# Kernel tuning notes

Measured on AMD Instinct MI355X. Metric: run time of the kernel, lower is better.

## Reference

```python
import jax, jax.numpy as jnp
import numpy as np

B, N, L, E, D = 16, 16384, 192, 128, 128


def setup_inputs() -> dict:
    key = jax.random.key(0)
    ks = jax.random.split(key, 16)
    s = 0.05
    return {
        "x_L_flattened": jax.random.normal(ks[0], (B, N), jnp.float32),
        "x_y_mask_flattened": jax.random.randint(ks[1], (B, N), 0, 2).astype(jnp.float32),
        "y_mask_L_flattened": jnp.zeros((B, N), jnp.float32),
        "x_y_mark": jax.random.normal(ks[2], (B, L, 1), jnp.float32),
        "variable_indices_flattened": jax.random.randint(ks[3], (B, N), 0, E),
        "time_indices_flattened": jax.random.randint(ks[4], (B, N), 0, L),
        "N_OBSERVATIONS_MAX": N,
        # learned params (stored [in, out]; torch Linear uses x @ W.T + b)
        "W_obs": jax.random.normal(ks[5], (2, D), jnp.float32) * s,
        "b_obs": jnp.zeros((D,), jnp.float32),
        "W_time": jax.random.normal(ks[6], (1, D), jnp.float32) * s,
        "b_time": jnp.zeros((D,), jnp.float32),
        "var_hyperedge_w": jax.random.normal(ks[7], (E, D), jnp.float32),
        "W_q": jax.random.normal(ks[8], (D, D), jnp.float32) * s,
        "b_q": jnp.zeros((D,), jnp.float32),
        "W_k": jax.random.normal(ks[9], (D, D), jnp.float32) * s,
        "b_k": jnp.zeros((D,), jnp.float32),
        "W_v": jax.random.normal(ks[10], (D, D), jnp.float32) * s,
        "b_v": jnp.zeros((D,), jnp.float32),
        "threshold": jnp.float32(0.5),
        "merge_coef": jnp.float32(0.5),
    }


def reference(x_L_flattened, x_y_mask_flattened, y_mask_L_flattened, x_y_mark,
              variable_indices_flattened, time_indices_flattened, N_OBSERVATIONS_MAX,
              W_obs, b_obs, W_time, b_time, var_hyperedge_w,
              W_q, b_q, W_k, b_k, W_v, b_v, threshold, merge_coef):
    mask = x_y_mask_flattened  # [B, N]
    # node features: value + (1 - mask + y_mask) channel -> [B, N, 2]
    feats = jnp.stack([x_L_flattened, 1.0 - mask + y_mask_L_flattened], axis=-1)
    # temporal incidence: node n belongs to time-edge l iff time_idx[n] == l; [B, L, N]
    ti = (time_indices_flattened[:, None, :] == jnp.arange(L)[None, :, None]).astype(jnp.float32)
    ti = ti * mask[:, None, :]
    # variable incidence: node n belongs to var-edge e iff var_idx[n] == e; [B, E, N]
    vi = (jnp.arange(E)[None, :, None] == variable_indices_flattened[:, None, :]).astype(jnp.float32)
    vi = vi * mask[:, None, :]
    # encoders
    obs = jax.nn.relu(feats @ W_obs + b_obs) * mask[..., None]          # [B, N, D]
    temp_he = jnp.sin(x_y_mark @ W_time + b_time)                        # [B, L, D]
    var_he = jax.nn.relu(jnp.broadcast_to(var_hyperedge_w, (B, E, D)))   # [B, E, D]
    # IrregularityAwareAttention over variable hyperedges with incidence as aux
    q = var_he @ W_q + b_q
    k = var_he @ W_k + b_k
    v = var_he @ W_v + b_v
    att = jnp.einsum('bed,bfd->bef', q, k) / (D ** 0.5)                  # [B, E, E]
    att_aux = jnp.einsum('ben,bfn->bef', vi, vi) / (N_OBSERVATIONS_MAX ** 0.5)
    merge = (att > threshold) & (att_aux != 0)
    att = jnp.where(merge, (1.0 - merge_coef) * att + merge_coef * att_aux, att)
    attn = jax.nn.softmax(att, axis=-1)
    out = jnp.einsum('bef,bfd->bed', attn, v)                            # [B, E, D]
    return (obs, temp_he, out, ti, vi)
```

## Files before the change

kernel.cpp:

```cpp
#include <hip/hip_runtime.h>

#define Bb 16
#define Nn 16384
#define Ll 192
#define Ee 128
#define Dd 128


__global__ __launch_bounds__(256) void k_main(
    const int* __restrict__ tidx, const int* __restrict__ vidx,
    const float* __restrict__ mask, const float* __restrict__ var_w,
    const float* __restrict__ Wq, const float* __restrict__ bq,
    const float* __restrict__ Wk, const float* __restrict__ bk,
    const float* __restrict__ Wv, const float* __restrict__ bv,
    const float* __restrict__ x, const float* __restrict__ ymask,
    const float* __restrict__ W_obs, const float* __restrict__ b_obs,
    const float* __restrict__ mark, const float* __restrict__ Wt,
    const float* __restrict__ bt,
    float* __restrict__ ti, float* __restrict__ vi,
    float* __restrict__ cnt_part,
    float* __restrict__ q, float* __restrict__ kT, float* __restrict__ v,
    float* __restrict__ obs, float* __restrict__ temp)
{
    __shared__ float sh[Ee];
    const int tid = threadIdx.x;

    if (blockIdx.x < 1024) {
        const int pb      = blockIdx.x >> 2;
        const int quarter = blockIdx.x & 3;
        const int g  = pb * 256 + tid;
        const int b  = g >> 12;
        const int n4 = (g & 4095) << 2;

        const int4   t4 = *reinterpret_cast<const int4*>(tidx + b * Nn + n4);
        const int4   v4 = *reinterpret_cast<const int4*>(vidx + b * Nn + n4);
        const float4 m4 = *reinterpret_cast<const float4*>(mask + b * Nn + n4);

        if (quarter == 0) {
            if (tid < Ee) sh[tid] = 0.0f;
            __syncthreads();
            if (m4.x != 0.0f) atomicAdd(&sh[v4.x], 1.0f);
            if (m4.y != 0.0f) atomicAdd(&sh[v4.y], 1.0f);
            if (m4.z != 0.0f) atomicAdd(&sh[v4.z], 1.0f);
            if (m4.w != 0.0f) atomicAdd(&sh[v4.w], 1.0f);
        }

        const int l0 = quarter * 48;
        float* tib = ti + (((size_t)b * Ll) << 14) + n4;
        #pragma unroll 4
        for (int l = l0; l < l0 + 48; ++l) {
            float4 o;
            o.x = (t4.x == l) ? m4.x : 0.0f;
            o.y = (t4.y == l) ? m4.y : 0.0f;
            o.z = (t4.z == l) ? m4.z : 0.0f;
            o.w = (t4.w == l) ? m4.w : 0.0f;
            *reinterpret_cast<float4*>(tib + ((size_t)l << 14)) = o;
        }

        const int e0 = quarter * 32;
        float* vib = vi + (((size_t)b * Ee) << 14) + n4;
        #pragma unroll 4
        for (int e = e0; e < e0 + 32; ++e) {
            float4 o;
            o.x = (v4.x == e) ? m4.x : 0.0f;
            o.y = (v4.y == e) ? m4.y : 0.0f;
            o.z = (v4.z == e) ? m4.z : 0.0f;
            o.w = (v4.w == e) ? m4.w : 0.0f;
            *reinterpret_cast<float4*>(vib + ((size_t)e << 14)) = o;
        }

        if (quarter == 0) {
            __syncthreads();
            if (tid < Ee) cnt_part[pb * Ee + tid] = sh[tid];
        }
    } else if (blockIdx.x < 1152) {
        const int e = blockIdx.x - 1024;
        const int d = tid;
        if (d < Dd) sh[d] = fmaxf(var_w[e * Dd + d], 0.0f);
        __syncthreads();
        if (d < Dd) {
            float aq = bq[d], ak = bk[d], av = bv[d];
            #pragma unroll 4
            for (int j = 0; j < Dd; ++j) {
                const float hj = sh[j];
                aq = fmaf(hj, Wq[j * Dd + d], aq);
                ak = fmaf(hj, Wk[j * Dd + d], ak);
                av = fmaf(hj, Wv[j * Dd + d], av);
            }
            q[e * Dd + d]  = aq;
            kT[d * Dd + e] = ak;
            v[e * Dd + d]  = av;
        }
    } else if (blockIdx.x < 33920) {
        const int g   = (blockIdx.x - 1152) * 256 + tid;
        const int row = g >> 5;
        const int d   = (g & 31) << 2;

        const float m  = mask[row];
        const float xv = x[row];
        const float f1 = 1.0f - m + ymask[row];

        const float4 w0 = *reinterpret_cast<const float4*>(W_obs + d);
        const float4 w1 = *reinterpret_cast<const float4*>(W_obs + Dd + d);
        const float4 bb = *reinterpret_cast<const float4*>(b_obs + d);

        float4 o;
        o.x = fmaxf(fmaf(xv, w0.x, fmaf(f1, w1.x, bb.x)), 0.0f) * m;
        o.y = fmaxf(fmaf(xv, w0.y, fmaf(f1, w1.y, bb.y)), 0.0f) * m;
        o.z = fmaxf(fmaf(xv, w0.z, fmaf(f1, w1.z, bb.z)), 0.0f) * m;
        o.w = fmaxf(fmaf(xv, w0.w, fmaf(f1, w1.w, bb.w)), 0.0f) * m;
        *reinterpret_cast<float4*>(obs + ((size_t)row << 7) + d) = o;
    } else {
        const int idx = (blockIdx.x - 33920) * 256 + tid;
        const int d = idx & 127;
        const int r = idx >> 7;
        temp[idx] = sinf(fmaf(mark[r], Wt[d], bt[d]));
    }
}

__global__ __launch_bounds__(128) void k_soft(
    const float* __restrict__ q, const float* __restrict__ kT,
    const float* __restrict__ v, const float* __restrict__ cnt_part,
    const float* __restrict__ thr_p, const float* __restrict__ mc_p,
    const int* __restrict__ nobs_p, float* __restrict__ outp)
{
    __shared__ float qr[Dd];
    __shared__ float attn[Ee];
    __shared__ float red[5];
    const int b = blockIdx.x >> 7;
    const int e = blockIdx.x & 127;
    const int f = threadIdx.x;

    qr[f] = q[e * Dd + f];

    float cp = (f < 16) ? cnt_part[(b * 16 + f) * Ee + e] : 0.0f;
    #pragma unroll
    for (int off = 8; off > 0; off >>= 1) cp += __shfl_xor(cp, off);
    if (f == 0) red[4] = cp;
    __syncthreads();

    float acc0 = 0.0f;
    #pragma unroll 4
    for (int d = 0; d < Dd; ++d) acc0 = fmaf(qr[d], kT[d * Dd + f], acc0);
    float a = acc0 * 0.08838834764831845f;

    if (f == e) {
        const float c = red[4];
        const float thr = *thr_p;
        if (c != 0.0f && a > thr) {
            const float mc  = *mc_p;
            const float aux = c / sqrtf((float)(*nobs_p));
            a = (1.0f - mc) * a + mc * aux;
        }
    }

    float mx = a;
    #pragma unroll
    for (int off = 32; off > 0; off >>= 1) mx = fmaxf(mx, __shfl_xor(mx, off));
    if ((f & 63) == 0) red[f >> 6] = mx;
    __syncthreads();
    mx = fmaxf(red[0], red[1]);

    const float ex = expf(a - mx);
    float s = ex;
    #pragma unroll
    for (int off = 32; off > 0; off >>= 1) s += __shfl_xor(s, off);
    if ((f & 63) == 0) red[2 + (f >> 6)] = s;
    __syncthreads();
    s = red[2] + red[3];

    attn[f] = ex / s;
    __syncthreads();

    const int d = f;
    float acc = 0.0f;
    #pragma unroll 4
    for (int j = 0; j < Ee; ++j) acc = fmaf(attn[j], v[j * Dd + d], acc);
    outp[((size_t)(b * Ee + e) << 7) + d] = acc;
}

extern "C" void kernel_launch(void* const* d_in, const int* in_sizes, int n_in,
                              void* d_out, int out_size, void* d_ws, size_t ws_size,
                              hipStream_t stream) {
    (void)in_sizes; (void)n_in; (void)out_size; (void)ws_size;

    const float* x      = (const float*)d_in[0];
    const float* mask   = (const float*)d_in[1];
    const float* ymask  = (const float*)d_in[2];
    const float* mark   = (const float*)d_in[3];
    const int*   vidx   = (const int*)d_in[4];
    const int*   tidx   = (const int*)d_in[5];
    const int*   nobs   = (const int*)d_in[6];
    const float* W_obs  = (const float*)d_in[7];
    const float* b_obs  = (const float*)d_in[8];
    const float* W_time = (const float*)d_in[9];
    const float* b_time = (const float*)d_in[10];
    const float* var_w  = (const float*)d_in[11];
    const float* W_q    = (const float*)d_in[12];
    const float* b_q    = (const float*)d_in[13];
    const float* W_k    = (const float*)d_in[14];
    const float* b_k    = (const float*)d_in[15];
    const float* W_v    = (const float*)d_in[16];
    const float* b_v    = (const float*)d_in[17];
    const float* thr    = (const float*)d_in[18];
    const float* mc     = (const float*)d_in[19];

    float* out_base = (float*)d_out;
    float* obs  = out_base;
    float* temp = out_base + 33554432;
    float* attO = out_base + 33947648;
    float* ti   = out_base + 34209792;
    float* vi   = out_base + 84541440;

    float* ws       = (float*)d_ws;
    float* cnt_part = ws;
    float* q        = ws + 32768;
    float* kT       = ws + 49152;
    float* v        = ws + 65536;

    k_main<<<35456, 256, 0, stream>>>(tidx, vidx, mask, var_w,
                                      W_q, b_q, W_k, b_k, W_v, b_v,
                                      x, ymask, W_obs, b_obs,
                                      mark, W_time, b_time,
                                      ti, vi, cnt_part, q, kT, v, obs, temp);
    k_soft<<<Bb * Ee, Dd, 0, stream>>>(q, kT, v, cnt_part, thr, mc, nobs, attO);
}
```

Baseline: 572.0 us.

## Replace dense one-hot incidence writes with bulk zero-fill plus sparse scatter

Instead of each thread computing and storing every compare-select entry of the ti and vi incidence matrices, the main kernel now zero-fills the contiguous ti+vi output region with wide coalesced stores. A separate scatter kernel then writes only the masked nonzero entries and computes the per-block variable counts. This aims to turn the dominant output traffic into a simple, well-parallelised memset and to spread it over many more blocks. In exchange it adds an extra kernel launch and a serial dependency, and it issues scattered 4-byte stores for the nonzeros.

Result: faster. 552.4 us (-3.4%).

```diff
diff --git a/kernel.cpp b/kernel.cpp
--- a/kernel.cpp
+++ b/kernel.cpp
@@ -7,92 +7,35 @@
 #define Dd 128
 
 
+#define QKV_NB   128
+#define TEMP_NB  1536
+#define FILL_NB  20480
+#define OBS_NB   32768
+#define TEMP_B0  (QKV_NB)
+#define FILL_B0  (TEMP_B0 + TEMP_NB)
+#define OBS_B0   (FILL_B0 + FILL_NB)
+#define GRID1    (OBS_B0 + OBS_NB)
+
 __global__ __launch_bounds__(256) void k_main(
-    const int* __restrict__ tidx, const int* __restrict__ vidx,
-    const float* __restrict__ mask, const float* __restrict__ var_w,
+    const float* __restrict__ var_w,
     const float* __restrict__ Wq, const float* __restrict__ bq,
     const float* __restrict__ Wk, const float* __restrict__ bk,
     const float* __restrict__ Wv, const float* __restrict__ bv,
-    const float* __restrict__ x, const float* __restrict__ ymask,
+    const float* __restrict__ x, const float* __restrict__ mask,
+    const float* __restrict__ ymask,
     const float* __restrict__ W_obs, const float* __restrict__ b_obs,
     const float* __restrict__ mark, const float* __restrict__ Wt,
     const float* __restrict__ bt,
-    float* __restrict__ ti, float* __restrict__ vi,
-    float* __restrict__ cnt_part,
+    float* __restrict__ zfill,
     float* __restrict__ q, float* __restrict__ kT, float* __restrict__ v,
     float* __restrict__ obs, float* __restrict__ temp)
 {
-    __shared__ float sh[Ee];
+    __shared__ float sh[Dd];
     const int tid = threadIdx.x;
-
-    if (blockIdx.x < 1024) {
-        const int pb      = blockIdx.x >> 2;
-        const int quarter = blockIdx.x & 3;
-        const int g  = pb * 256 + tid;
-        const int b  = g >> 12;
-        const int n4 = (g & 4095) << 2;
-
-        const int4   t4 = *reinterpret_cast<const int4*>(tidx + b * Nn + n4);
-        const int4   v4 = *reinterpret_cast<const int4*>(vidx + b * Nn + n4);
-        const float4 m4 = *reinterpret_cast<const float4*>(mask + b * Nn + n4);
-
-        if (quarter == 0) {
-            if (tid < Ee) sh[tid] = 0.0f;
-            __syncthreads();
-            if (m4.x != 0.0f) atomicAdd(&sh[v4.x], 1.0f);
-            if (m4.y != 0.0f) atomicAdd(&sh[v4.y], 1.0f);
-            if (m4.z != 0.0f) atomicAdd(&sh[v4.z], 1.0f);
-            if (m4.w != 0.0f) atomicAdd(&sh[v4.w], 1.0f);
-        }
-
-        const int l0 = quarter * 48;
-        float* tib = ti + (((size_t)b * Ll) << 14) + n4;
-        #pragma unroll 4
-        for (int l = l0; l < l0 + 48; ++l) {
-            float4 o;
-            o.x = (t4.x == l) ? m4.x : 0.0f;
-            o.y = (t4.y == l) ? m4.y : 0.0f;
-            o.z = (t4.z == l) ? m4.z : 0.0f;
-            o.w = (t4.w == l) ? m4.w : 0.0f;
-            *reinterpret_cast<float4*>(tib + ((size_t)l << 14)) = o;
-        }
-
-        const int e0 = quarter * 32;
-        float* vib = vi + (((size_t)b * Ee) << 14) + n4;
-        #pragma unroll 4
-        for (int e = e0; e < e0 + 32; ++e) {
-            float4 o;
-            o.x = (v4.x == e) ? m4.x : 0.0f;
-            o.y = (v4.y == e) ? m4.y : 0.0f;
-            o.z = (v4.z == e) ? m4.z : 0.0f;
-            o.w = (v4.w == e) ? m4.w : 0.0f;
-            *reinterpret_cast<float4*>(vib + ((size_t)e << 14)) = o;
-        }
-
-        if (quarter == 0) {
-            __syncthreads();
-            if (tid < Ee) cnt_part[pb * Ee + tid] = sh[tid];
-        }
-    } else if (blockIdx.x < 1152) {
-        const int e = blockIdx.x - 1024;
-        const int d = tid;
-        if (d < Dd) sh[d] = fmaxf(var_w[e * Dd + d], 0.0f);
-        __syncthreads();
-        if (d < Dd) {
-            float aq = bq[d], ak = bk[d], av = bv[d];
-            #pragma unroll 4
-            for (int j = 0; j < Dd; ++j) {
-                const float hj = sh[j];
-                aq = fmaf(hj, Wq[j * Dd + d], aq);
-                ak = fmaf(hj, Wk[j * Dd + d], ak);
-                av = fmaf(hj, Wv[j * Dd + d], av);
-            }
-            q[e * Dd + d]  = aq;
-            kT[d * Dd + e] = ak;
-            v[e * Dd + d]  = av;
-        }
-    } else if (blockIdx.x < 33920) {
-        const int g   = (blockIdx.x - 1152) * 256 + tid;
+    const unsigned bx = blockIdx.x;
+
+    if (bx >= OBS_B0) {
+        const int g   = (bx - OBS_B0) * 256 + tid;
         const int row = g >> 5;
         const int d   = (g & 31) << 2;
 
@@ -110,12 +53,84 @@
         o.z = fmaxf(fmaf(xv, w0.z, fmaf(f1, w1.z, bb.z)), 0.0f) * m;
         o.w = fmaxf(fmaf(xv, w0.w, fmaf(f1, w1.w, bb.w)), 0.0f) * m;
         *reinterpret_cast<float4*>(obs + ((size_t)row << 7) + d) = o;
-    } else {
-        const int idx = (blockIdx.x - 33920) * 256 + tid;
+    } else if (bx >= FILL_B0) {
+        float4* p = reinterpret_cast<float4*>(zfill)
+                  + ((size_t)(bx - FILL_B0) << 10) + tid;
+        const float4 z = make_float4(0.0f, 0.0f, 0.0f, 0.0f);
+        p[0]   = z;
+        p[256] = z;
+        p[512] = z;
+        p[768] = z;
+    } else if (bx >= TEMP_B0) {
+        const int idx = (bx - TEMP_B0) * 256 + tid;
         const int d = idx & 127;
         const int r = idx >> 7;
         temp[idx] = sinf(fmaf(mark[r], Wt[d], bt[d]));
-    }
+    } else {
+        const int e = bx;
+        if (tid < Dd) sh[tid] = fmaxf(var_w[e * Dd + tid], 0.0f);
+        __syncthreads();
+        if (tid < Dd) {
+            float aq = bq[tid], ak = bk[tid], av = bv[tid];
+            #pragma unroll 4
+            for (int j = 0; j < Dd; ++j) {
+                const float hj = sh[j];
+                aq = fmaf(hj, Wq[j * Dd + tid], aq);
+                ak = fmaf(hj, Wk[j * Dd + tid], ak);
+                av = fmaf(hj, Wv[j * Dd + tid], av);
+            }
+            q[e * Dd + tid]  = aq;
+            kT[tid * Dd + e] = ak;
+            v[e * Dd + tid]  = av;
+        }
+    }
+}
+
+__global__ __launch_bounds__(256) void k_scatter(
+    const int* __restrict__ tidx, const int* __restrict__ vidx,
+    const float* __restrict__ mask,
+    float* __restrict__ ti, float* __restrict__ vi,
+    float* __restrict__ cnt_part)
+{
+    __shared__ float sh[Ee];
+    const int tid = threadIdx.x;
+    const int g  = blockIdx.x * 256 + tid;
+    const int b  = g >> 12;
+    const int n4 = (g & 4095) << 2;
+
+    const int4   t4 = *reinterpret_cast<const int4*>(tidx + b * Nn + n4);
+    const int4   v4 = *reinterpret_cast<const int4*>(vidx + b * Nn + n4);
+    const float4 m4 = *reinterpret_cast<const float4*>(mask + b * Nn + n4);
+
+    if (tid < Ee) sh[tid] = 0.0f;
+    __syncthreads();
+
+    float* tib = ti + (((size_t)b * Ll) << 14);
+    float* vib = vi + (((size_t)b * Ee) << 14);
+
+    if (m4.x != 0.0f) {
+        atomicAdd(&sh[v4.x], 1.0f);
+        tib[((size_t)t4.x << 14) + n4]     = m4.x;
+        vib[((size_t)v4.x << 14) + n4]     = m4.x;
+    }
+    if (m4.y != 0.0f) {
+        atomicAdd(&sh[v4.y], 1.0f);
+        tib[((size_t)t4.y << 14) + n4 + 1] = m4.y;
+        vib[((size_t)v4.y << 14) + n4 + 1] = m4.y;
+    }
+    if (m4.z != 0.0f) {
+        atomicAdd(&sh[v4.z], 1.0f);
+        tib[((size_t)t4.z << 14) + n4 + 2] = m4.z;
+        vib[((size_t)v4.z << 14) + n4 + 2] = m4.z;
+    }
+    if (m4.w != 0.0f) {
+        atomicAdd(&sh[v4.w], 1.0f);
+        tib[((size_t)t4.w << 14) + n4 + 3] = m4.w;
+        vib[((size_t)v4.w << 14) + n4 + 3] = m4.w;
+    }
+
+    __syncthreads();
+    if (tid < Ee) cnt_part[blockIdx.x * Ee + tid] = sh[tid];
 }
 
 __global__ __launch_bounds__(128) void k_soft(
@@ -218,10 +233,12 @@
     float* kT       = ws + 49152;
     float* v        = ws + 65536;
 
-    k_main<<<35456, 256, 0, stream>>>(tidx, vidx, mask, var_w,
+    k_main<<<GRID1, 256, 0, stream>>>(var_w,
                                       W_q, b_q, W_k, b_k, W_v, b_v,
-                                      x, ymask, W_obs, b_obs,
+                                      x, mask, ymask, W_obs, b_obs,
                                       mark, W_time, b_time,
-                                      ti, vi, cnt_part, q, kT, v, obs, temp);
+                                      ti ,
+                                      q, kT, v, obs, temp);
+    k_scatter<<<256, 256, 0, stream>>>(tidx, vidx, mask, ti, vi, cnt_part);
     k_soft<<<Bb * Ee, Dd, 0, stream>>>(q, kT, v, cnt_part, thr, mc, nobs, attO);
 }
```
